# Kernel tuning notes

Measured on AMD Instinct MI355X. Metric: run time of the kernel, lower is better.

## Reference

```python
import jax, jax.numpy as jnp
import numpy as np

# Static problem sizes (must match input construction)
B, G, EPG, K, C = 64, 24, 512, 20, 1
NS = B * G            # total number of subgraphs
E = NS * EPG          # total number of edges
M, H = 4096, 256      # node_state shape


def setup_inputs() -> dict:
    key = jax.random.key(0)
    ks = jax.random.split(key, 8)
    label = (jax.random.uniform(ks[0], (E,)) < 0.5).astype(jnp.float32)
    label0 = (jax.random.uniform(ks[1], (E,)) < 0.5).astype(jnp.float32)
    log_theta = jax.random.normal(ks[2], (E, K), dtype=jnp.float32)
    log_theta0 = jax.random.normal(ks[3], (E, K), dtype=jnp.float32)
    log_alpha = jax.random.normal(ks[4], (E, K), dtype=jnp.float32)
    log_alpha0 = jax.random.normal(ks[5], (E, K), dtype=jnp.float32)
    subgraph_idx = (jnp.arange(E, dtype=jnp.int32) // EPG).astype(jnp.int32)
    subgraph_idx0 = subgraph_idx
    subgraph_idx_base = (jnp.arange(B + 1, dtype=jnp.int32) * (G * C)).astype(jnp.int32)
    subgraph_idx_base0 = subgraph_idx_base
    node_state = jax.random.normal(ks[6], (M, H), dtype=jnp.float32)
    node_state0 = jax.random.normal(ks[7], (M, H), dtype=jnp.float32)
    return {
        "label": label, "label0": label0,
        "log_theta": log_theta, "log_theta0": log_theta0,
        "log_alpha": log_alpha, "log_alpha0": log_alpha0,
        "subgraph_idx": subgraph_idx, "subgraph_idx0": subgraph_idx0,
        "subgraph_idx_base": subgraph_idx_base, "subgraph_idx_base0": subgraph_idx_base0,
        "node_state": node_state, "node_state0": node_state0,
    }


def _bce_with_logits(logits, y):
    # BCEWithLogitsLoss(reduction='none'), broadcast label over K mixture components
    return -(y[:, None] * jax.nn.log_sigmoid(logits)
             + (1.0 - y)[:, None] * jax.nn.log_sigmoid(-logits))


def _stream_loss(label, log_theta, log_alpha, subgraph_idx, subgraph_idx_base):
    adj_loss = _bce_with_logits(log_theta, label)                     # E x K
    const = jax.ops.segment_sum(jnp.ones((E,), jnp.float32), subgraph_idx, NS)  # edges per subgraph
    reduce_adj_loss = jax.ops.segment_sum(adj_loss, subgraph_idx, NS)  # NS x K
    reduce_log_alpha = jax.ops.segment_sum(log_alpha, subgraph_idx, NS) / const[:, None]
    reduce_log_alpha = jax.nn.log_softmax(reduce_log_alpha, axis=-1)
    log_prob = jax.nn.logsumexp(-reduce_adj_loss + reduce_log_alpha, axis=1)  # NS
    # bc_idx: map each subgraph to its (batch, canonical-order) slot; C == 1 here,
    # equivalent to repeat_interleave(arange(B*C), bc_size) in the original.
    bc_idx = jnp.searchsorted(subgraph_idx_base, jnp.arange(NS, dtype=jnp.int32), side='right') - 1
    bc_log_prob = jax.ops.segment_sum(log_prob, bc_idx, B * C).reshape(B, C)
    bc_const = jax.ops.segment_sum(const, bc_idx, B * C).reshape(B, C)
    bc_loss = bc_log_prob / bc_const
    b_loss = jax.nn.logsumexp(bc_loss, axis=1)   # sum_order_log_prob=False
    return jnp.mean(-b_loss)                      # reduction='mean'


def _trace_cdist(ns, ns0):
    # Fused replacement for the naive O(m^2) host-side pairwise-distance loop:
    # D[i,j] = ||ns[i] - ns0[j]||, then trace(D).
    x2 = jnp.sum(ns * ns, axis=1)
    y2 = jnp.sum(ns0 * ns0, axis=1)
    d2 = x2[:, None] + y2[None, :] - 2.0 * (ns @ ns0.T)   # M x M
    D = jnp.sqrt(jnp.maximum(d2, 0.0))
    return jnp.trace(D)


def reference(label, label0, log_theta, log_theta0, log_alpha, log_alpha0,
              subgraph_idx, subgraph_idx0, subgraph_idx_base, subgraph_idx_base0,
              node_state, node_state0):
    loss = _stream_loss(label, log_theta, log_alpha, subgraph_idx, subgraph_idx_base)
    loss0 = _stream_loss(label0, log_theta0, log_alpha0, subgraph_idx0, subgraph_idx_base0)
    trD = _trace_cdist(node_state, node_state0)
    # return_neg_log_prob=False branch of the original
    return 10.0 * (loss + loss0) + trD
```

## Files before the change

### kernel.cpp

```cpp
#include <hip/hip_runtime.h>
#include <math.h>

#define B_   64
#define G_   24
#define EPG_ 512
#define K_   20
#define NS_  (B_ * G_)
#define E_   (NS_ * EPG_)
#define M_   4096
#define H_   256

#define NT_  320
#define F4_  (EPG_ * K_ / 4)
#define IT_  (F4_ / NT_)

#define CD_ROWS_   20
#define CD_BLOCKS_ ((M_ + CD_ROWS_ - 1) / CD_ROWS_)

__device__ __forceinline__ float bce_f(float x, float y) {
    return fmaxf(x, 0.f) - x * y + __logf(1.f + __expf(-fabsf(x)));
}

__global__ __launch_bounds__(NT_, 4)
void fused_kernel(const float* __restrict__ label,
                  const float* __restrict__ label0,
                  const float* __restrict__ log_theta,
                  const float* __restrict__ log_theta0,
                  const float* __restrict__ log_alpha,
                  const float* __restrict__ log_alpha0,
                  const float* __restrict__ ns,
                  const float* __restrict__ ns0,
                  float* __restrict__ out)
{
    __shared__ float  s_lab[2][EPG_];
    __shared__ float4 red_adj[2][NT_];
    __shared__ float4 red_alpha[2][NT_];
    __shared__ float  S_red[2][2][K_];
    __shared__ float  s_lp[2];
    __shared__ float  s_cd[5];

    const int tid = threadIdx.x;

    if (blockIdx.x < CD_BLOCKS_) {
        const int wave = tid >> 6, lane = tid & 63;
        float acc = 0.f;
        #pragma unroll
        for (int i = 0; i < 4; ++i) {
            const int row = blockIdx.x * CD_ROWS_ + wave * 4 + i;
            if (row < M_) {
                const float4 a = ((const float4*)(ns  + (size_t)row * H_))[lane];
                const float4 b = ((const float4*)(ns0 + (size_t)row * H_))[lane];
                const float dx = a.x - b.x, dy = a.y - b.y;
                const float dz = a.z - b.z, dw = a.w - b.w;
                float sv = dx * dx + dy * dy + dz * dz + dw * dw;
                #pragma unroll
                for (int off = 32; off > 0; off >>= 1) sv += __shfl_down(sv, off);
                if (lane == 0) acc += sqrtf(sv);
            }
        }
        if (lane == 0) s_cd[wave] = acc;
        __syncthreads();
        if (tid == 0)
            atomicAdd(out, s_cd[0] + s_cd[1] + s_cd[2] + s_cd[3] + s_cd[4]);
        return;
    }

    const int s = blockIdx.x - CD_BLOCKS_;

    const float4* t0 = (const float4*)log_theta  + (size_t)s * F4_;
    const float4* t1 = (const float4*)log_theta0 + (size_t)s * F4_;
    const float4* a0 = (const float4*)log_alpha  + (size_t)s * F4_;
    const float4* a1 = (const float4*)log_alpha0 + (size_t)s * F4_;

    float4 lv;
    if (tid < 128)      lv = ((const float4*)(label  + (size_t)s * EPG_))[tid];
    else if (tid < 256) lv = ((const float4*)(label0 + (size_t)s * EPG_))[tid - 128];

    float4 cx0 = t0[tid], cx1 = t1[tid], ca0 = a0[tid], ca1 = a1[tid];

    if (tid < 128)      ((float4*)&s_lab[0][0])[tid]       = lv;
    else if (tid < 256) ((float4*)&s_lab[1][0])[tid - 128] = lv;
    __syncthreads();

    const int e_div = tid / 5;
    float4 AJ0 = {0,0,0,0}, AJ1 = {0,0,0,0}, AL0 = {0,0,0,0}, AL1 = {0,0,0,0};

    #pragma unroll
    for (int i = 0; i < IT_; ++i) {
        float4 nx0 = cx0, nx1 = cx1, na0 = ca0, na1 = ca1;
        if (i + 1 < IT_) {
            const int f = (i + 1) * NT_ + tid;
            nx0 = t0[f]; nx1 = t1[f]; na0 = a0[f]; na1 = a1[f];
        }
        const float y0 = s_lab[0][i * 64 + e_div];
        const float y1 = s_lab[1][i * 64 + e_div];
        AJ0.x += bce_f(cx0.x, y0); AJ0.y += bce_f(cx0.y, y0);
        AJ0.z += bce_f(cx0.z, y0); AJ0.w += bce_f(cx0.w, y0);
        AJ1.x += bce_f(cx1.x, y1); AJ1.y += bce_f(cx1.y, y1);
        AJ1.z += bce_f(cx1.z, y1); AJ1.w += bce_f(cx1.w, y1);
        AL0.x += ca0.x; AL0.y += ca0.y; AL0.z += ca0.z; AL0.w += ca0.w;
        AL1.x += ca1.x; AL1.y += ca1.y; AL1.z += ca1.z; AL1.w += ca1.w;
        cx0 = nx0; cx1 = nx1; ca0 = na0; ca1 = na1;
    }

    red_adj[0][tid]   = AJ0;  red_adj[1][tid]   = AJ1;
    red_alpha[0][tid] = AL0;  red_alpha[1][tid] = AL1;
    __syncthreads();

    {
        const int g = tid >> 2, sub = tid & 3;
        const int st = g / 40, r = g % 40, which = r / 20, k = r % 20;
        const int q = k >> 2, j = k & 3;
        const float* basep = which ? (const float*)&red_alpha[st][0]
                                   : (const float*)&red_adj[st][0];
        float v = 0.f;
        #pragma unroll
        for (int mm = 0; mm < 16; ++mm) {
            const int t = q + 20 * mm + 5 * sub;
            v += basep[t * 4 + j];
        }
        v += __shfl_down(v, 2);
        v += __shfl_down(v, 1);
        if (sub == 0) S_red[st][which][k] = v;
    }
    __syncthreads();

    if (tid == 0 || tid == 64) {
        const int st = tid >> 6;
        const float inv_c = 1.0f / (float)EPG_;
        float va[K_];
        #pragma unroll
        for (int k = 0; k < K_; ++k) va[k] = S_red[st][1][k] * inv_c;
        float m1 = -INFINITY;
        #pragma unroll
        for (int k = 0; k < K_; ++k) m1 = fmaxf(m1, va[k]);
        float s1 = 0.f;
        #pragma unroll
        for (int k = 0; k < K_; ++k) s1 += __expf(va[k] - m1);
        const float lse = m1 + __logf(s1);

        float w[K_];
        float m2 = -INFINITY;
        #pragma unroll
        for (int k = 0; k < K_; ++k) {
            w[k] = va[k] - lse - S_red[st][0][k];
            m2 = fmaxf(m2, w[k]);
        }
        float s2 = 0.f;
        #pragma unroll
        for (int k = 0; k < K_; ++k) s2 += __expf(w[k] - m2);
        s_lp[st] = m2 + __logf(s2);
    }
    __syncthreads();
    if (tid == 0)
        atomicAdd(out, (s_lp[0] + s_lp[1]) * (-10.0f / (float)E_));
}

extern "C" void kernel_launch(void* const* d_in, const int* in_sizes, int n_in,
                              void* d_out, int out_size, void* d_ws, size_t ws_size,
                              hipStream_t stream) {
    const float* label       = (const float*)d_in[0];
    const float* label0      = (const float*)d_in[1];
    const float* log_theta   = (const float*)d_in[2];
    const float* log_theta0  = (const float*)d_in[3];
    const float* log_alpha   = (const float*)d_in[4];
    const float* log_alpha0  = (const float*)d_in[5];
    const float* node_state  = (const float*)d_in[10];
    const float* node_state0 = (const float*)d_in[11];
    float* out = (float*)d_out;

    hipMemsetAsync(out, 0, sizeof(float), stream);

    fused_kernel<<<dim3(CD_BLOCKS_ + NS_), NT_, 0, stream>>>(
        label, label0, log_theta, log_theta0, log_alpha, log_alpha0,
        node_state, node_state0, out);
}
```

Measured before the change: 264.1 us.

## Split subgraph loss into interleaved grid-strided accumulation and separate finish kernel

```diff
diff --git a/kernel.cpp b/kernel.cpp
--- a/kernel.cpp
+++ b/kernel.cpp
@@ -9,44 +9,47 @@
 #define E_   (NS_ * EPG_)
 #define M_   4096
 #define H_   256
+#define F4_  (EPG_ * K_ / 4)
 
-#define NT_  320
-#define F4_  (EPG_ * K_ / 4)
-#define IT_  (F4_ / NT_)
+#define NB1_ 1536
+#define NT1_ 320
+#define T1_  (NB1_ * NT1_)
+#define NV_  8
+#define SPV_ (T1_ / F4_)
 
 #define CD_ROWS_   20
 #define CD_BLOCKS_ ((M_ + CD_ROWS_ - 1) / CD_ROWS_)
+
+#define WS_FLOATS_ (2 * 2 * NS_ * K_)
 
 __device__ __forceinline__ float bce_f(float x, float y) {
     return fmaxf(x, 0.f) - x * y + __logf(1.f + __expf(-fabsf(x)));
 }
 
-__global__ __launch_bounds__(NT_, 4)
-void fused_kernel(const float* __restrict__ label,
+__global__ __launch_bounds__(NT1_)
+void accum_kernel(const float* __restrict__ label,
                   const float* __restrict__ label0,
-                  const float* __restrict__ log_theta,
-                  const float* __restrict__ log_theta0,
-                  const float* __restrict__ log_alpha,
-                  const float* __restrict__ log_alpha0,
+                  const float4* __restrict__ gt,
+                  const float4* __restrict__ gt0,
+                  const float4* __restrict__ ga,
+                  const float4* __restrict__ ga0,
                   const float* __restrict__ ns,
                   const float* __restrict__ ns0,
+                  float* __restrict__ ws,
                   float* __restrict__ out)
 {
-    __shared__ float  s_lab[2][EPG_];
-    __shared__ float4 red_adj[2][NT_];
-    __shared__ float4 red_alpha[2][NT_];
-    __shared__ float  S_red[2][2][K_];
-    __shared__ float  s_lp[2];
+    __shared__ float4 s_red[4][NT1_];
     __shared__ float  s_cd[5];
 
     const int tid = threadIdx.x;
 
-    if (blockIdx.x < CD_BLOCKS_) {
+    if (blockIdx.x >= NB1_) {
+        const int cb = blockIdx.x - NB1_;
         const int wave = tid >> 6, lane = tid & 63;
         float acc = 0.f;
         #pragma unroll
         for (int i = 0; i < 4; ++i) {
-            const int row = blockIdx.x * CD_ROWS_ + wave * 4 + i;
+            const int row = cb * CD_ROWS_ + wave * 4 + i;
             if (row < M_) {
                 const float4 a = ((const float4*)(ns  + (size_t)row * H_))[lane];
                 const float4 b = ((const float4*)(ns0 + (size_t)row * H_))[lane];
@@ -65,95 +68,91 @@
         return;
     }
 
-    const int s = blockIdx.x - CD_BLOCKS_;
+    const int b    = blockIdx.x;
+    const int sgrp = b >> 3;
 
-    const float4* t0 = (const float4*)log_theta  + (size_t)s * F4_;
-    const float4* t1 = (const float4*)log_theta0 + (size_t)s * F4_;
-    const float4* a0 = (const float4*)log_alpha  + (size_t)s * F4_;
-    const float4* a1 = (const float4*)log_alpha0 + (size_t)s * F4_;
-
-    float4 lv;
-    if (tid < 128)      lv = ((const float4*)(label  + (size_t)s * EPG_))[tid];
-    else if (tid < 256) lv = ((const float4*)(label0 + (size_t)s * EPG_))[tid - 128];
-
-    float4 cx0 = t0[tid], cx1 = t1[tid], ca0 = a0[tid], ca1 = a1[tid];
-
-    if (tid < 128)      ((float4*)&s_lab[0][0])[tid]       = lv;
-    else if (tid < 256) ((float4*)&s_lab[1][0])[tid - 128] = lv;
-    __syncthreads();
-
-    const int e_div = tid / 5;
-    float4 AJ0 = {0,0,0,0}, AJ1 = {0,0,0,0}, AL0 = {0,0,0,0}, AL1 = {0,0,0,0};
-
-    #pragma unroll
-    for (int i = 0; i < IT_; ++i) {
-        float4 nx0 = cx0, nx1 = cx1, na0 = ca0, na1 = ca1;
-        if (i + 1 < IT_) {
-            const int f = (i + 1) * NT_ + tid;
-            nx0 = t0[f]; nx1 = t1[f]; na0 = a0[f]; na1 = a1[f];
-        }
-        const float y0 = s_lab[0][i * 64 + e_div];
-        const float y1 = s_lab[1][i * 64 + e_div];
-        AJ0.x += bce_f(cx0.x, y0); AJ0.y += bce_f(cx0.y, y0);
-        AJ0.z += bce_f(cx0.z, y0); AJ0.w += bce_f(cx0.w, y0);
-        AJ1.x += bce_f(cx1.x, y1); AJ1.y += bce_f(cx1.y, y1);
-        AJ1.z += bce_f(cx1.z, y1); AJ1.w += bce_f(cx1.w, y1);
-        AL0.x += ca0.x; AL0.y += ca0.y; AL0.z += ca0.z; AL0.w += ca0.w;
-        AL1.x += ca1.x; AL1.y += ca1.y; AL1.z += ca1.z; AL1.w += ca1.w;
-        cx0 = nx0; cx1 = nx1; ca0 = na0; ca1 = na1;
-    }
-
-    red_adj[0][tid]   = AJ0;  red_adj[1][tid]   = AJ1;
-    red_alpha[0][tid] = AL0;  red_alpha[1][tid] = AL1;
-    __syncthreads();
+    const int g   = tid >> 2, sub = tid & 3;
+    const int qt  = g / 20,  k   = g % 20;
+    const int q   = k >> 2,  j   = k & 3;
+    const float* basep = (const float*)&s_red[qt][0];
+    const int ws_base = (((qt >> 1) * 2 + (qt & 1)) * NS_) * K_ + k;
 
     {
-        const int g = tid >> 2, sub = tid & 3;
-        const int st = g / 40, r = g % 40, which = r / 20, k = r % 20;
-        const int q = k >> 2, j = k & 3;
-        const float* basep = which ? (const float*)&red_alpha[st][0]
-                                   : (const float*)&red_adj[st][0];
-        float v = 0.f;
-        #pragma unroll
-        for (int mm = 0; mm < 16; ++mm) {
-            const int t = q + 20 * mm + 5 * sub;
-            v += basep[t * 4 + j];
+        const size_t f = (size_t)b * NT1_ + tid;
+        const int    e = b * 64 + tid / 5;
+        float4 x0 = gt[f], x1 = gt0[f], c0 = ga[f], c1 = ga0[f];
+        float  y0 = label[e], y1 = label0[e];
+
+        for (int v = 0; v < NV_; ++v) {
+            float4 nx0, nx1, nc0, nc1; float ny0, ny1;
+            if (v + 1 < NV_) {
+                const size_t fn = (size_t)(v + 1) * T1_ + (size_t)b * NT1_ + tid;
+                const int    en = (v + 1) * (T1_ / 5) + b * 64 + tid / 5;
+                nx0 = gt[fn]; nx1 = gt0[fn]; nc0 = ga[fn]; nc1 = ga0[fn];
+                ny0 = label[en]; ny1 = label0[en];
+            }
+
+            float4 J0, J1;
+            J0.x = bce_f(x0.x, y0); J0.y = bce_f(x0.y, y0);
+            J0.z = bce_f(x0.z, y0); J0.w = bce_f(x0.w, y0);
+            J1.x = bce_f(x1.x, y1); J1.y = bce_f(x1.y, y1);
+            J1.z = bce_f(x1.z, y1); J1.w = bce_f(x1.w, y1);
+            s_red[0][tid] = J0;  s_red[1][tid] = J1;
+            s_red[2][tid] = c0;  s_red[3][tid] = c1;
+            __syncthreads();
+
+            {
+                float vsum = 0.f;
+                #pragma unroll
+                for (int mm = 0; mm < 16; ++mm)
+                    vsum += basep[(q + 20 * mm + 5 * sub) * 4 + j];
+                vsum += __shfl_down(vsum, 2);
+                vsum += __shfl_down(vsum, 1);
+                if (sub == 0) {
+                    const int s = v * SPV_ + sgrp;
+                    atomicAdd(&ws[ws_base + s * K_], vsum);
+                }
+            }
+            __syncthreads();
+
+            x0 = nx0; x1 = nx1; c0 = nc0; c1 = nc1; y0 = ny0; y1 = ny1;
         }
-        v += __shfl_down(v, 2);
-        v += __shfl_down(v, 1);
-        if (sub == 0) S_red[st][which][k] = v;
     }
-    __syncthreads();
+}
 
-    if (tid == 0 || tid == 64) {
-        const int st = tid >> 6;
-        const float inv_c = 1.0f / (float)EPG_;
-        float va[K_];
-        #pragma unroll
-        for (int k = 0; k < K_; ++k) va[k] = S_red[st][1][k] * inv_c;
-        float m1 = -INFINITY;
-        #pragma unroll
-        for (int k = 0; k < K_; ++k) m1 = fmaxf(m1, va[k]);
-        float s1 = 0.f;
-        #pragma unroll
-        for (int k = 0; k < K_; ++k) s1 += __expf(va[k] - m1);
-        const float lse = m1 + __logf(s1);
+__global__ __launch_bounds__(256)
+void finish_kernel(const float* __restrict__ ws, float* __restrict__ out)
+{
+    const int gid = blockIdx.x * 256 + threadIdx.x;
+    const int st = gid & 1, s = gid >> 1;
+    const float* Wadj = ws + ((0 * 2 + st) * NS_ + s) * K_;
+    const float* Walp = ws + ((1 * 2 + st) * NS_ + s) * K_;
 
-        float w[K_];
-        float m2 = -INFINITY;
-        #pragma unroll
-        for (int k = 0; k < K_; ++k) {
-            w[k] = va[k] - lse - S_red[st][0][k];
-            m2 = fmaxf(m2, w[k]);
-        }
-        float s2 = 0.f;
-        #pragma unroll
-        for (int k = 0; k < K_; ++k) s2 += __expf(w[k] - m2);
-        s_lp[st] = m2 + __logf(s2);
+    const float inv_c = 1.0f / (float)EPG_;
+    float va[K_];
+    #pragma unroll
+    for (int kk = 0; kk < K_; ++kk) va[kk] = Walp[kk] * inv_c;
+    float m1 = -INFINITY;
+    #pragma unroll
+    for (int kk = 0; kk < K_; ++kk) m1 = fmaxf(m1, va[kk]);
+    float s1 = 0.f;
+    #pragma unroll
+    for (int kk = 0; kk < K_; ++kk) s1 += __expf(va[kk] - m1);
+    const float lse = m1 + __logf(s1);
+
+    float w[K_];
+    float m2 = -INFINITY;
+    #pragma unroll
+    for (int kk = 0; kk < K_; ++kk) {
+        w[kk] = va[kk] - lse - Wadj[kk];
+        m2 = fmaxf(m2, w[kk]);
     }
-    __syncthreads();
-    if (tid == 0)
-        atomicAdd(out, (s_lp[0] + s_lp[1]) * (-10.0f / (float)E_));
+    float s2 = 0.f;
+    #pragma unroll
+    for (int kk = 0; kk < K_; ++kk) s2 += __expf(w[kk] - m2);
+    const float lp = m2 + __logf(s2);
+
+    atomicAdd(out, lp * (-10.0f / (float)E_));
 }
 
 extern "C" void kernel_launch(void* const* d_in, const int* in_sizes, int n_in,
@@ -168,10 +167,16 @@
     const float* node_state  = (const float*)d_in[10];
     const float* node_state0 = (const float*)d_in[11];
     float* out = (float*)d_out;
+    float* ws  = (float*)d_ws;
 
     hipMemsetAsync(out, 0, sizeof(float), stream);
+    hipMemsetAsync(ws, 0, WS_FLOATS_ * sizeof(float), stream);
 
-    fused_kernel<<<dim3(CD_BLOCKS_ + NS_), NT_, 0, stream>>>(
-        label, label0, log_theta, log_theta0, log_alpha, log_alpha0,
-        node_state, node_state0, out);
+    accum_kernel<<<dim3(NB1_ + CD_BLOCKS_), NT1_, 0, stream>>>(
+        label, label0,
+        (const float4*)log_theta, (const float4*)log_theta0,
+        (const float4*)log_alpha, (const float4*)log_alpha0,
+        node_state, node_state0, ws, out);
+
+    finish_kernel<<<dim3(12), 256, 0, stream>>>(ws, out);
 }
```

New measurement: 272.3 us. 1.03x slower.
